# Performance work log

Measured on AMD Instinct MI355X. Metric: run time of the kernel, lower is better.

The kernel has to match this reference:

```python
import jax, jax.numpy as jnp
import numpy as np


def ste_sign(x):
    # larq ste_sign forward: sign(x) with sign(0) = 1
    return jnp.where(x >= 0, 1.0, -1.0).astype(x.dtype)


def setup_inputs() -> dict:
    key = jax.random.key(0)
    ks = jax.random.split(key, 8)
    B, H, W, Cin, Cout = 32, 56, 56, 256, 256
    x = jax.random.normal(ks[0], (B, H, W, Cin), dtype=jnp.float32)
    bias1 = jax.random.normal(ks[1], (1, 1, 1, Cin), dtype=jnp.float32) * 0.01
    kernel = jax.random.normal(ks[2], (3, 3, Cin, Cout), dtype=jnp.float32) * 0.1
    # BatchNormalization(scale=False): beta learnable, gamma=1, moving stats
    bn_beta = jax.random.normal(ks[3], (Cout,), dtype=jnp.float32) * 0.01
    bn_mean = jax.random.normal(ks[4], (Cout,), dtype=jnp.float32) * 0.01
    bn_var = jax.random.uniform(ks[5], (Cout,), dtype=jnp.float32, minval=0.5, maxval=1.5)
    bias2 = jax.random.normal(ks[6], (1, 1, 1, Cout), dtype=jnp.float32) * 0.01
    return {"x": x, "bias1": bias1, "kernel": kernel, "bn_beta": bn_beta,
            "bn_mean": bn_mean, "bn_var": bn_var, "bias2": bias2}


def reference(x, bias1, kernel, bn_beta, bn_mean, bn_var, bias2):
    eps = 1e-3  # keras BatchNormalization default epsilon
    strides = 1
    # lb_activation_1: learnable bias + ste_sign activation
    a = ste_sign(x + bias1)
    # QuantConv2D: binarize kernel, 'same' padding conv (NHWC, HWIO)
    qk = ste_sign(kernel)
    y = jax.lax.conv_general_dilated(
        a, qk, window_strides=(strides, strides), padding='SAME',
        dimension_numbers=('NHWC', 'HWIO', 'NHWC'))
    # BatchNormalization(scale=False) inference: (y - mean)/sqrt(var+eps) + beta
    y = (y - bn_mean) * jax.lax.rsqrt(bn_var + eps) + bn_beta
    # strides == 1: no avgpool residual branch
    # lb_activation_2: learnable bias + relu
    out = jax.nn.relu(y + bias2)
    return out
```

## Files before the change

kernel.cpp:

```cpp
#include <hip/hip_runtime.h>


typedef int v4i __attribute__((ext_vector_type(4)));
typedef unsigned int u32;

#define NB   32
#define HW   56
#define HP   58
#define HP2  (HP*HP)
#define CIN  256
#define COUT 256
#define NPIX (NB*HW*HW)
#define KTOT 2304
#define BM   128
#define NSTEP 36

#define PA_BYTES ((size_t)NB*HP*HP*CIN)
#define WT_OFF   PA_BYTES
#define WT_BYTES ((size_t)KTOT*COUT)
#define SC_OFF   (WT_OFF + WT_BYTES)
#define SH_OFF   (SC_OFF + 1024)

__device__ __forceinline__ void g2l16(const void* g, void* l) {
    __builtin_amdgcn_global_load_lds(
        (const __attribute__((address_space(1))) void*)g,
        (__attribute__((address_space(3))) void*)l, 16, 0, 0);
}

__global__ __launch_bounds__(256) void pack_a_kernel(
    const float* __restrict__ x, const float* __restrict__ b1,
    signed char* __restrict__ pa)
{
    const int lane = threadIdx.x & 63;
    const int pp = blockIdx.x * 4 + (threadIdx.x >> 6);
    const int n = pp / HP2, r = pp % HP2, ph = r / HP, pw = r % HP;
    const int ci = lane * 4;
    u32 o = 0;
    if (ph >= 1 && ph <= HW && pw >= 1 && pw <= HW) {
        const int pix = (n * HW + ph - 1) * HW + (pw - 1);
        const float4 xv = *(const float4*)(x + (size_t)pix * CIN + ci);
        const float4 bv = *(const float4*)(b1 + ci);
        o  = (u32)(unsigned char)((xv.x + bv.x >= 0.f) ? 1 : -1);
        o |= (u32)(unsigned char)((xv.y + bv.y >= 0.f) ? 1 : -1) << 8;
        o |= (u32)(unsigned char)((xv.z + bv.z >= 0.f) ? 1 : -1) << 16;
        o |= (u32)(unsigned char)((xv.w + bv.w >= 0.f) ? 1 : -1) << 24;
    }
    *(u32*)(pa + (size_t)pp * CIN + ci) = o;
}

__global__ __launch_bounds__(256) void packw_kernel(
    const float* __restrict__ k, signed char* __restrict__ wt)
{
    __shared__ signed char tile[64][256];
    const int t = threadIdx.x, k0 = blockIdx.x * 64;
    for (int j = 0; j < 64; ++j)
        tile[j][t] = (k[(size_t)(k0 + j) * COUT + t] >= 0.f) ? 1 : -1;
    __syncthreads();
    u32 wd[16];
#pragma unroll
    for (int j = 0; j < 16; ++j) wd[j] = 0;
#pragma unroll
    for (int j = 0; j < 64; ++j)
        wd[j >> 2] |= ((u32)(unsigned char)tile[j][t]) << ((j & 3) * 8);
    uint4* dst = (uint4*)(wt + (size_t)t * KTOT + k0);
#pragma unroll
    for (int j = 0; j < 4; ++j)
        dst[j] = make_uint4(wd[4*j], wd[4*j+1], wd[4*j+2], wd[4*j+3]);
}

__global__ __launch_bounds__(256) void bnprep_kernel(
    const float* __restrict__ beta, const float* __restrict__ mean,
    const float* __restrict__ var, const float* __restrict__ b2,
    float* __restrict__ scale, float* __restrict__ shift)
{
    const int t = threadIdx.x;
    const float s = rsqrtf(var[t] + 1e-3f);
    scale[t] = s;
    shift[t] = beta[t] - mean[t] * s + b2[t];
}

__global__ __launch_bounds__(256, 2) void conv_mfma_kernel(
    const signed char* __restrict__ pa, const signed char* __restrict__ wt,
    const float* __restrict__ scale, const float* __restrict__ shift,
    float* __restrict__ out)
{
    __shared__ signed char Al[3][BM * 64];
    __shared__ signed char Bl[3][COUT * 64];

    const int t = threadIdx.x, l = t & 63, v = t >> 6;
    const int p0 = blockIdx.x * BM;

    const signed char* abase[2];
#pragma unroll
    for (int i = 0; i < 2; ++i) {
        const int q = (t >> 2) + i * 64;
        const int p = p0 + q;
        const int n = p / 3136, r = p % 3136, h = r / 56, w = r % 56;
        const int aswz = (((t & 3) ^ ((q >> 1) & 3)) << 4);
        abase[i] = pa + ((size_t)(n * HP + h) * HP + w) * CIN + aswz;
    }

    const signed char* wbase[4];
#pragma unroll
    for (int j = 0; j < 4; ++j) {
        const int co = v * 64 + j * 16 + (l >> 2);
        const int bswz = (((l & 3) ^ ((co >> 1) & 3)) << 4);
        wbase[j] = wt + (size_t)co * KTOT + bswz;
    }

    int aoff[8], boff[4];
#pragma unroll
    for (int pg = 0; pg < 8; ++pg) {
        const int row = pg * 16 + (l & 15);
        aoff[pg] = row * 64 + ((((l >> 4) ^ (row >> 1)) & 3) << 4);
    }
#pragma unroll
    for (int cg = 0; cg < 4; ++cg) {
        const int row = v * 64 + cg * 16 + (l & 15);
        boff[cg] = row * 64 + ((((l >> 4) ^ (row >> 1)) & 3) << 4);
    }

    v4i acc[8][4];
#pragma unroll
    for (int i = 0; i < 8; ++i)
#pragma unroll
        for (int j = 0; j < 4; ++j) acc[i][j] = (v4i){0, 0, 0, 0};

    auto STAGE = [&](int buf, int s) {
        const int tap = s >> 2, cq = s & 3;
        const int ty = tap / 3, tx = tap - ty * 3;
        const int goff = ((ty * HP + tx) << 8) + (cq << 6);
        g2l16(abase[0] + goff, &Al[buf][v * 1024]);
        g2l16(abase[1] + goff, &Al[buf][4096 + v * 1024]);
#pragma unroll
        for (int j = 0; j < 4; ++j)
            g2l16(wbase[j] + (s << 6), &Bl[buf][v * 4096 + j * 1024]);
    };
    auto COMPUTE = [&](int cur) {
        v4i af[8], bf[4];
#pragma unroll
        for (int pg = 0; pg < 8; ++pg) af[pg] = *(const v4i*)(&Al[cur][aoff[pg]]);
#pragma unroll
        for (int cg = 0; cg < 4; ++cg) bf[cg] = *(const v4i*)(&Bl[cur][boff[cg]]);
#pragma unroll
        for (int pg = 0; pg < 8; ++pg)
#pragma unroll
            for (int cg = 0; cg < 4; ++cg)
                acc[pg][cg] = __builtin_amdgcn_mfma_i32_16x16x64_i8(
                    af[pg], bf[cg], acc[pg][cg], 0, 0, 0);
    };

    STAGE(0, 0);
    STAGE(1, 1);
#pragma unroll 1
    for (int s = 0; s < NSTEP - 2; ++s) {
        STAGE((s + 2) % 3, s + 2);
        asm volatile("s_waitcnt vmcnt(12)" ::: "memory");
        __builtin_amdgcn_s_barrier();
        asm volatile("" ::: "memory");
        COMPUTE(s % 3);
        asm volatile("" ::: "memory");
        __builtin_amdgcn_s_barrier();
        asm volatile("" ::: "memory");
    }
    asm volatile("s_waitcnt vmcnt(6)" ::: "memory");
    __builtin_amdgcn_s_barrier();
    asm volatile("" ::: "memory");
    COMPUTE((NSTEP - 2) % 3);
    asm volatile("s_waitcnt vmcnt(0)" ::: "memory");
    __builtin_amdgcn_s_barrier();
    asm volatile("" ::: "memory");
    COMPUTE((NSTEP - 1) % 3);

#pragma unroll
    for (int cg = 0; cg < 4; ++cg) {
        const int co = v * 64 + cg * 16 + (l & 15);
        const float sc = scale[co], sh = shift[co];
#pragma unroll
        for (int pg = 0; pg < 8; ++pg) {
            const int prow0 = p0 + pg * 16 + (l >> 4) * 4;
#pragma unroll
            for (int rr = 0; rr < 4; ++rr) {
                const float y = (float)acc[pg][cg][rr];
                out[(size_t)(prow0 + rr) * COUT + co] = fmaxf(fmaf(y, sc, sh), 0.f);
            }
        }
    }
}

extern "C" void kernel_launch(void* const* d_in, const int* in_sizes, int n_in,
                              void* d_out, int out_size, void* d_ws, size_t ws_size,
                              hipStream_t stream)
{
    const float* x      = (const float*)d_in[0];
    const float* bias1  = (const float*)d_in[1];
    const float* kernel = (const float*)d_in[2];
    const float* bn_beta = (const float*)d_in[3];
    const float* bn_mean = (const float*)d_in[4];
    const float* bn_var  = (const float*)d_in[5];
    const float* bias2   = (const float*)d_in[6];
    float* out = (float*)d_out;

    signed char* pa  = (signed char*)d_ws;
    signed char* wtp = (signed char*)d_ws + WT_OFF;
    float* scale = (float*)((char*)d_ws + SC_OFF);
    float* shift = (float*)((char*)d_ws + SH_OFF);

    pack_a_kernel<<<dim3(NB * HP2 / 4), dim3(256), 0, stream>>>(x, bias1, pa);
    packw_kernel<<<dim3(KTOT / 64), dim3(256), 0, stream>>>(kernel, wtp);
    bnprep_kernel<<<dim3(1), dim3(256), 0, stream>>>(bn_beta, bn_mean, bn_var, bias2,
                                                     scale, shift);
    conv_mfma_kernel<<<dim3(NPIX / BM), dim3(256), 0, stream>>>(pa, wtp, scale, shift, out);
}
```

Baseline: 123.1 us.

## Split each K-step into two interleaved load/MFMA phases with priority hints

The main loop is restructured so each K-step runs as two half-phases. Each half reads its LDS fragments, issues part of the next stage's global-to-LDS copies, then runs 16 MFMAs under raised wave priority (s_setprio). The goal is to spread the memory issue across the compute and keep the matrix units busy instead of issuing all loads and then all MFMAs. The cost is two extra barriers per step and a more delicate vmcnt accounting for the three-buffer ring.

```diff
diff --git a/kernel.cpp b/kernel.cpp
--- a/kernel.cpp
+++ b/kernel.cpp
@@ -126,51 +126,100 @@
 #pragma unroll
         for (int j = 0; j < 4; ++j) acc[i][j] = (v4i){0, 0, 0, 0};
 
-    auto STAGE = [&](int buf, int s) {
+    auto goffA = [&](int s) {
         const int tap = s >> 2, cq = s & 3;
         const int ty = tap / 3, tx = tap - ty * 3;
-        const int goff = ((ty * HP + tx) << 8) + (cq << 6);
-        g2l16(abase[0] + goff, &Al[buf][v * 1024]);
-        g2l16(abase[1] + goff, &Al[buf][4096 + v * 1024]);
-#pragma unroll
-        for (int j = 0; j < 4; ++j)
+        return ((ty * HP + tx) << 8) + (cq << 6);
+    };
+    auto STAGE_P0 = [&](int buf, int s) {
+        const int go = goffA(s);
+        g2l16(abase[0] + go, &Al[buf][v * 1024]);
+        g2l16(abase[1] + go, &Al[buf][4096 + v * 1024]);
+        g2l16(wbase[0] + (s << 6), &Bl[buf][v * 4096]);
+    };
+    auto STAGE_P1 = [&](int buf, int s) {
+#pragma unroll
+        for (int j = 1; j < 4; ++j)
             g2l16(wbase[j] + (s << 6), &Bl[buf][v * 4096 + j * 1024]);
     };
-    auto COMPUTE = [&](int cur) {
-        v4i af[8], bf[4];
-#pragma unroll
-        for (int pg = 0; pg < 8; ++pg) af[pg] = *(const v4i*)(&Al[cur][aoff[pg]]);
-#pragma unroll
-        for (int cg = 0; cg < 4; ++cg) bf[cg] = *(const v4i*)(&Bl[cur][boff[cg]]);
-#pragma unroll
-        for (int pg = 0; pg < 8; ++pg)
-#pragma unroll
-            for (int cg = 0; cg < 4; ++cg)
-                acc[pg][cg] = __builtin_amdgcn_mfma_i32_16x16x64_i8(
-                    af[pg], bf[cg], acc[pg][cg], 0, 0, 0);
-    };
-
-    STAGE(0, 0);
-    STAGE(1, 1);
-#pragma unroll 1
-    for (int s = 0; s < NSTEP - 2; ++s) {
-        STAGE((s + 2) % 3, s + 2);
-        asm volatile("s_waitcnt vmcnt(12)" ::: "memory");
-        __builtin_amdgcn_s_barrier();
-        asm volatile("" ::: "memory");
-        COMPUTE(s % 3);
-        asm volatile("" ::: "memory");
-        __builtin_amdgcn_s_barrier();
-        asm volatile("" ::: "memory");
-    }
+
+    STAGE_P0(0, 0); STAGE_P1(0, 0);
+    STAGE_P0(1, 1); STAGE_P1(1, 1);
     asm volatile("s_waitcnt vmcnt(6)" ::: "memory");
     __builtin_amdgcn_s_barrier();
-    asm volatile("" ::: "memory");
-    COMPUTE((NSTEP - 2) % 3);
-    asm volatile("s_waitcnt vmcnt(0)" ::: "memory");
-    __builtin_amdgcn_s_barrier();
-    asm volatile("" ::: "memory");
-    COMPUTE((NSTEP - 1) % 3);
+
+    int cur = 0;
+#pragma unroll 1
+    for (int s = 0; s < NSTEP; ++s) {
+        signed char* Ac = &Al[0][0] + cur * (BM * 64);
+        signed char* Bc = &Bl[0][0] + cur * (COUT * 64);
+        const int stg = (cur >= 1) ? cur - 1 : 2;
+        const bool do_stage = (s + 2 < NSTEP);
+
+        v4i af0 = *(const v4i*)(Ac + aoff[0]);
+        v4i af1 = *(const v4i*)(Ac + aoff[1]);
+        v4i af2 = *(const v4i*)(Ac + aoff[2]);
+        v4i af3 = *(const v4i*)(Ac + aoff[3]);
+        v4i bf0 = *(const v4i*)(Bc + boff[0]);
+        v4i bf1 = *(const v4i*)(Bc + boff[1]);
+        v4i bf2 = *(const v4i*)(Bc + boff[2]);
+        v4i bf3 = *(const v4i*)(Bc + boff[3]);
+        if (do_stage) STAGE_P0(stg, s + 2);
+        asm volatile("" ::: "memory");
+        __builtin_amdgcn_s_barrier();
+        __builtin_amdgcn_s_setprio(1);
+        acc[0][0] = __builtin_amdgcn_mfma_i32_16x16x64_i8(af0, bf0, acc[0][0], 0, 0, 0);
+        acc[0][1] = __builtin_amdgcn_mfma_i32_16x16x64_i8(af0, bf1, acc[0][1], 0, 0, 0);
+        acc[0][2] = __builtin_amdgcn_mfma_i32_16x16x64_i8(af0, bf2, acc[0][2], 0, 0, 0);
+        acc[0][3] = __builtin_amdgcn_mfma_i32_16x16x64_i8(af0, bf3, acc[0][3], 0, 0, 0);
+        acc[1][0] = __builtin_amdgcn_mfma_i32_16x16x64_i8(af1, bf0, acc[1][0], 0, 0, 0);
+        acc[1][1] = __builtin_amdgcn_mfma_i32_16x16x64_i8(af1, bf1, acc[1][1], 0, 0, 0);
+        acc[1][2] = __builtin_amdgcn_mfma_i32_16x16x64_i8(af1, bf2, acc[1][2], 0, 0, 0);
+        acc[1][3] = __builtin_amdgcn_mfma_i32_16x16x64_i8(af1, bf3, acc[1][3], 0, 0, 0);
+        acc[2][0] = __builtin_amdgcn_mfma_i32_16x16x64_i8(af2, bf0, acc[2][0], 0, 0, 0);
+        acc[2][1] = __builtin_amdgcn_mfma_i32_16x16x64_i8(af2, bf1, acc[2][1], 0, 0, 0);
+        acc[2][2] = __builtin_amdgcn_mfma_i32_16x16x64_i8(af2, bf2, acc[2][2], 0, 0, 0);
+        acc[2][3] = __builtin_amdgcn_mfma_i32_16x16x64_i8(af2, bf3, acc[2][3], 0, 0, 0);
+        acc[3][0] = __builtin_amdgcn_mfma_i32_16x16x64_i8(af3, bf0, acc[3][0], 0, 0, 0);
+        acc[3][1] = __builtin_amdgcn_mfma_i32_16x16x64_i8(af3, bf1, acc[3][1], 0, 0, 0);
+        acc[3][2] = __builtin_amdgcn_mfma_i32_16x16x64_i8(af3, bf2, acc[3][2], 0, 0, 0);
+        acc[3][3] = __builtin_amdgcn_mfma_i32_16x16x64_i8(af3, bf3, acc[3][3], 0, 0, 0);
+        __builtin_amdgcn_s_setprio(0);
+        asm volatile("" ::: "memory");
+        __builtin_amdgcn_s_barrier();
+
+        v4i af4 = *(const v4i*)(Ac + aoff[4]);
+        v4i af5 = *(const v4i*)(Ac + aoff[5]);
+        v4i af6 = *(const v4i*)(Ac + aoff[6]);
+        v4i af7 = *(const v4i*)(Ac + aoff[7]);
+        if (do_stage) STAGE_P1(stg, s + 2);
+        asm volatile("" ::: "memory");
+        __builtin_amdgcn_s_barrier();
+        __builtin_amdgcn_s_setprio(1);
+        acc[4][0] = __builtin_amdgcn_mfma_i32_16x16x64_i8(af4, bf0, acc[4][0], 0, 0, 0);
+        acc[4][1] = __builtin_amdgcn_mfma_i32_16x16x64_i8(af4, bf1, acc[4][1], 0, 0, 0);
+        acc[4][2] = __builtin_amdgcn_mfma_i32_16x16x64_i8(af4, bf2, acc[4][2], 0, 0, 0);
+        acc[4][3] = __builtin_amdgcn_mfma_i32_16x16x64_i8(af4, bf3, acc[4][3], 0, 0, 0);
+        acc[5][0] = __builtin_amdgcn_mfma_i32_16x16x64_i8(af5, bf0, acc[5][0], 0, 0, 0);
+        acc[5][1] = __builtin_amdgcn_mfma_i32_16x16x64_i8(af5, bf1, acc[5][1], 0, 0, 0);
+        acc[5][2] = __builtin_amdgcn_mfma_i32_16x16x64_i8(af5, bf2, acc[5][2], 0, 0, 0);
+        acc[5][3] = __builtin_amdgcn_mfma_i32_16x16x64_i8(af5, bf3, acc[5][3], 0, 0, 0);
+        acc[6][0] = __builtin_amdgcn_mfma_i32_16x16x64_i8(af6, bf0, acc[6][0], 0, 0, 0);
+        acc[6][1] = __builtin_amdgcn_mfma_i32_16x16x64_i8(af6, bf1, acc[6][1], 0, 0, 0);
+        acc[6][2] = __builtin_amdgcn_mfma_i32_16x16x64_i8(af6, bf2, acc[6][2], 0, 0, 0);
+        acc[6][3] = __builtin_amdgcn_mfma_i32_16x16x64_i8(af6, bf3, acc[6][3], 0, 0, 0);
+        acc[7][0] = __builtin_amdgcn_mfma_i32_16x16x64_i8(af7, bf0, acc[7][0], 0, 0, 0);
+        acc[7][1] = __builtin_amdgcn_mfma_i32_16x16x64_i8(af7, bf1, acc[7][1], 0, 0, 0);
+        acc[7][2] = __builtin_amdgcn_mfma_i32_16x16x64_i8(af7, bf2, acc[7][2], 0, 0, 0);
+        acc[7][3] = __builtin_amdgcn_mfma_i32_16x16x64_i8(af7, bf3, acc[7][3], 0, 0, 0);
+        __builtin_amdgcn_s_setprio(0);
+
+        if (s + 2 < NSTEP)      { asm volatile("s_waitcnt vmcnt(6)" ::: "memory"); }
+        else if (s + 1 < NSTEP) { asm volatile("s_waitcnt vmcnt(0)" ::: "memory"); }
+        asm volatile("" ::: "memory");
+        __builtin_amdgcn_s_barrier();
+        cur = (cur >= 2) ? 0 : cur + 1;
+    }
 
 #pragma unroll
     for (int cg = 0; cg < 4; ++cg) {
```

Result: faster. 110.7 us (-10.1%).
